# Optimization experiments

Measured on AMD Instinct MI355X. Metric: run time of the kernel, lower is better.

The kernel has to match this reference:

```python
import jax, jax.numpy as jnp
import numpy as np

B, C, Q, E, H = 8, 1024, 128, 512, 1024


def setup_inputs() -> dict:
    key = jax.random.key(0)
    ks = jax.random.split(key, 8)
    return {
        "context": jax.random.normal(ks[0], (B, C, E), jnp.float32),
        "question": jax.random.normal(ks[1], (B, Q, E), jnp.float32),
        "context_mask": jnp.ones((B, C), jnp.float32),
        "w_question": jax.random.normal(ks[2], (E,), jnp.float32),
        "w_context": jax.random.normal(ks[3], (E,), jnp.float32),
        "w_multiple": jax.random.normal(ks[4], (E,), jnp.float32),
        "W1": jax.random.normal(ks[5], (4 * E, H), jnp.float32) * 0.02,
        "b1": jnp.zeros((H,), jnp.float32),
        "W2": jax.random.normal(ks[6], (H, 4 * E), jnp.float32) * 0.02,
        "b2": jnp.zeros((4 * E,), jnp.float32),
    }


def reference(context, question, context_mask, w_question, w_context, w_multiple, W1, b1, W2, b2):
    # Dropout is identity at eval time.
    # Trilinear similarity: s[b,c,q] = q.w_q + ctx.w_c + sum_e q_e*ctx_e*w_m_e
    q_w = question @ w_question                                  # (B,Q)
    c_w = context @ w_context                                    # (B,C)
    mult = jnp.einsum("bqe,bce->bcq", question * w_multiple, context)  # avoids (B,C,Q,E)
    sim = q_w[:, None, :] + c_w[:, :, None] + mult               # (B,C,Q)

    # Context2Query: softmax over question dim (dim=2)
    c2q = jnp.einsum("bcq,bqe->bce", jax.nn.softmax(sim, axis=2), question)
    # Query2Context: max over question dim, softmax over context dim (dim=1)
    q2c = jnp.einsum("bc,bce->be", jax.nn.softmax(jnp.max(sim, axis=2), axis=1), context)  # (B,E)

    attended = jnp.concatenate(
        [context, c2q, context * c2q, context * q2c[:, None, :]], axis=2
    )  # (B,C,4E)

    # MaskedLinear: linear then zero out masked context positions
    m = context_mask[:, :, None]
    h = (attended @ W1 + b1) * m
    out = jax.nn.relu((h @ W2 + b2) * m)
    return out
```

## Files before the change

### kernel.cpp

```cpp
#include <hip/hip_runtime.h>

typedef __bf16 bf16;
typedef __bf16 bf16x2 __attribute__((ext_vector_type(2)));
typedef __bf16 bf16x4 __attribute__((ext_vector_type(4)));
typedef __bf16 bf16x8 __attribute__((ext_vector_type(8)));
typedef float f32x4 __attribute__((ext_vector_type(4)));

#define AS1 __attribute__((address_space(1)))
#define AS3 __attribute__((address_space(3)))

__device__ __forceinline__ void async_copy16(const void* g, void* l) {
  __builtin_amdgcn_global_load_lds((const AS1 void*)g, (AS3 void*)l, 16, 0, 0);
}

#define BB 8
#define CC 1024
#define QQ 128
#define EE 512
#define HH 1024
#define FOURE 2048

__global__ __launch_bounds__(256) void prep_kernel(
    const float* __restrict__ W1, const float* __restrict__ W2,
    const float* __restrict__ qst, const float* __restrict__ wmul,
    const float* __restrict__ wqv, bf16* __restrict__ W1T,
    bf16* __restrict__ W2T, bf16* __restrict__ qT,
    bf16* __restrict__ qmh, bf16* __restrict__ qml, float* __restrict__ qw,
    float* __restrict__ q2c) {
  __shared__ float tile[32][33];
  __shared__ float r4[4];
  int bx = blockIdx.x;
  int t = threadIdx.x;
  if (bx >= 5120) {
    for (int i = t; i < BB * EE; i += 256) q2c[i] = 0.f;
    return;
  }
  if (bx >= 4608) {
    int i = bx - 4608;
    int half = t >> 7, tr = t & 127;
    int rowg = i * 2 + half;
    const float* qrow = qst + (size_t)rowg * EE;
    float4 qv = *(const float4*)&qrow[tr * 4];
    float4 wm4 = *(const float4*)&wmul[tr * 4];
    float4 wq4 = *(const float4*)&wqv[tr * 4];
    float m[4] = {qv.x * wm4.x, qv.y * wm4.y, qv.z * wm4.z, qv.w * wm4.w};
    bf16x4 h, l;
#pragma unroll
    for (int k = 0; k < 4; ++k) {
      bf16 hh = (bf16)m[k];
      h[k] = hh; l[k] = (bf16)(m[k] - (float)hh);
    }
    *(bf16x4*)&qmh[(size_t)rowg * EE + tr * 4] = h;
    *(bf16x4*)&qml[(size_t)rowg * EE + tr * 4] = l;
    float s = qv.x * wq4.x + qv.y * wq4.y + qv.z * wq4.z + qv.w * wq4.w;
#pragma unroll
    for (int off = 32; off; off >>= 1) s += __shfl_xor(s, off);
    if ((t & 63) == 0) r4[t >> 6] = s;
    __syncthreads();
    if (tr == 0) qw[rowg] = r4[half * 2] + r4[half * 2 + 1];
    return;
  }
  const float* src;
  bf16* dst;
  int R, C, idx;
  if (bx < 2048) {
    src = W1; dst = W1T; R = 2048; C = 1024; idx = bx;
  } else if (bx < 4096) {
    src = W2; dst = W2T; R = 1024; C = 2048; idx = bx - 2048;
  } else {
    int i = bx - 4096;
    int b = i >> 6; idx = i & 63;
    src = qst + (size_t)b * QQ * EE; dst = qT + (size_t)b * EE * QQ;
    R = 128; C = 512;
  }
  int ctiles = C >> 5;
  int by = idx / ctiles, cx = idx % ctiles;
  int tx = t & 31, ty = t >> 5;
#pragma unroll
  for (int rr = 0; rr < 4; ++rr)
    tile[ty + rr * 8][tx] = src[(size_t)(by * 32 + ty + rr * 8) * C + cx * 32 + tx];
  __syncthreads();
#pragma unroll
  for (int rr = 0; rr < 4; ++rr)
    dst[(size_t)(cx * 32 + ty + rr * 8) * R + by * 32 + tx] = (bf16)tile[tx][ty + rr * 8];
}

__global__ __launch_bounds__(256) void fused_att_kernel(
    const float* __restrict__ ctx, const bf16* __restrict__ qmh,
    const bf16* __restrict__ qml, const bf16* __restrict__ qT,
    const float* __restrict__ wc, const float* __restrict__ qw,
    float* __restrict__ smax, bf16* __restrict__ att) {
  int bid = blockIdx.x;
  int b = bid & 7;
  int m0 = (bid >> 3) * 16;
  __shared__ __align__(16) char U[26880];
  bf16* Ah = (bf16*)(U);
  bf16* Al = (bf16*)(U + 1024);
  bf16* Bh = (bf16*)(U + 2048);
  bf16* Bl = (bf16*)(U + 10240);
  float(*sim_s)[132] = (float(*)[132])(U + 18432);
  bf16* c2q_lds = (bf16*)(U);
  __shared__ float wc_s[EE];
  __shared__ float qw_s[QQ];
  __shared__ float cw_s[16];
  __shared__ bf16 P_lds[16][136];
  int t = threadIdx.x;
  for (int i = t; i < EE; i += 256) wc_s[i] = wc[i];
  if (t < QQ) qw_s[t] = qw[b * QQ + t];
  __syncthreads();
  int wv = t >> 6, ln = t & 63;
  int rl = ln & 15, kq = ln >> 4;
  f32x4 acc[2] = {};
  const float* Ag = ctx + ((size_t)b * CC + m0) * EE;
  const bf16* Bhg = qmh + (size_t)b * QQ * EE;
  const bf16* Blg = qml + (size_t)b * QQ * EE;
  int arow = t >> 4, ae = (t & 15) * 2;
  float cwp = 0.f;
  for (int k0 = 0; k0 < EE; k0 += 32) {
    {
      float2 v = *(const float2*)(Ag + (size_t)arow * EE + k0 + ae);
      cwp += v.x * wc_s[k0 + ae] + v.y * wc_s[k0 + ae + 1];
      bf16 h0 = (bf16)v.x, h1 = (bf16)v.y;
      bf16x2 h, l;
      h[0] = h0; h[1] = h1;
      l[0] = (bf16)(v.x - (float)h0);
      l[1] = (bf16)(v.y - (float)h1);
      int sl = ((ae >> 3) ^ ((arow >> 1) & 3)) * 8 + (ae & 7);
      *(bf16x2*)&Ah[arow * 32 + sl] = h;
      *(bf16x2*)&Al[arow * 32 + sl] = l;
    }
#pragma unroll
    for (int r = 0; r < 2; ++r) {
      int fb = (r * 4 + wv) * 1024 + ln * 16;
      int row = fb >> 6;
      int cq = ((fb >> 4) & 3) ^ ((row >> 1) & 3);
      async_copy16(Bhg + (size_t)row * EE + k0 + cq * 8, (char*)Bh + fb);
      async_copy16(Blg + (size_t)row * EE + k0 + cq * 8, (char*)Bl + fb);
    }
    __syncthreads();
    bf16x8 ah, al, bh[2], bl[2];
    {
      int sl = (kq ^ ((rl >> 1) & 3)) * 8;
      ah = *(const bf16x8*)&Ah[rl * 32 + sl];
      al = *(const bf16x8*)&Al[rl * 32 + sl];
    }
#pragma unroll
    for (int j = 0; j < 2; ++j) {
      int r = wv * 32 + j * 16 + rl;
      int sl = (kq ^ ((r >> 1) & 3)) * 8;
      bh[j] = *(const bf16x8*)&Bh[r * 32 + sl];
      bl[j] = *(const bf16x8*)&Bl[r * 32 + sl];
    }
#pragma unroll
    for (int j = 0; j < 2; ++j) {
      acc[j] = __builtin_amdgcn_mfma_f32_16x16x32_bf16(ah, bh[j], acc[j], 0, 0, 0);
      acc[j] = __builtin_amdgcn_mfma_f32_16x16x32_bf16(ah, bl[j], acc[j], 0, 0, 0);
      acc[j] = __builtin_amdgcn_mfma_f32_16x16x32_bf16(al, bh[j], acc[j], 0, 0, 0);
    }
    __syncthreads();
  }
  {
    float s = cwp;
    s += __shfl_xor(s, 1); s += __shfl_xor(s, 2);
    s += __shfl_xor(s, 4); s += __shfl_xor(s, 8);
    if ((t & 15) == 0) cw_s[arow] = s;
  }
#pragma unroll
  for (int j = 0; j < 2; ++j) {
    int col = wv * 32 + j * 16 + rl;
    float qv = qw_s[col];
    int rbase = kq * 4;
#pragma unroll
    for (int r = 0; r < 4; ++r) sim_s[rbase + r][col] = acc[j][r] + qv;
  }
  __syncthreads();
  {
    int row = t >> 4, cb = t & 15;
    float v[8];
    float mx = -3.4e38f;
#pragma unroll
    for (int k = 0; k < 8; ++k) {
      v[k] = sim_s[row][cb + 16 * k];
      mx = fmaxf(mx, v[k]);
    }
    mx = fmaxf(mx, __shfl_xor(mx, 1));
    mx = fmaxf(mx, __shfl_xor(mx, 2));
    mx = fmaxf(mx, __shfl_xor(mx, 4));
    mx = fmaxf(mx, __shfl_xor(mx, 8));
    float sm = 0.f;
#pragma unroll
    for (int k = 0; k < 8; ++k) { v[k] = __expf(v[k] - mx); sm += v[k]; }
    sm += __shfl_xor(sm, 1);
    sm += __shfl_xor(sm, 2);
    sm += __shfl_xor(sm, 4);
    sm += __shfl_xor(sm, 8);
    float inv = 1.0f / sm;
#pragma unroll
    for (int k = 0; k < 8; ++k) P_lds[row][cb + 16 * k] = (bf16)(v[k] * inv);
    if (cb == 0) smax[b * CC + m0 + row] = mx + cw_s[row];
  }
  __syncthreads();
  f32x4 acc2[8] = {};
  const bf16* qTb = qT + (size_t)b * EE * QQ;
#pragma unroll
  for (int kk = 0; kk < 4; ++kk) {
    bf16x8 af2;
    {
      bf16x4 lo = *(const bf16x4*)&P_lds[rl][kk * 32 + kq * 8];
      bf16x4 hi = *(const bf16x4*)&P_lds[rl][kk * 32 + kq * 8 + 4];
      af2[0] = lo[0]; af2[1] = lo[1]; af2[2] = lo[2]; af2[3] = lo[3];
      af2[4] = hi[0]; af2[5] = hi[1]; af2[6] = hi[2]; af2[7] = hi[3];
    }
#pragma unroll
    for (int j = 0; j < 8; ++j) {
      int n = wv * 128 + j * 16 + rl;
      bf16x8 bfr = *(const bf16x8*)&qTb[(size_t)n * QQ + kk * 32 + kq * 8];
      acc2[j] = __builtin_amdgcn_mfma_f32_16x16x32_bf16(af2, bfr, acc2[j], 0, 0, 0);
    }
  }
#pragma unroll
  for (int j = 0; j < 8; ++j) {
    int col = wv * 128 + j * 16 + rl;
    int rbase = kq * 4;
#pragma unroll
    for (int r = 0; r < 4; ++r)
      c2q_lds[(size_t)(rbase + r) * 520 + col] = (bf16)acc2[j][r];
  }
  __syncthreads();
  {
    int row = t >> 4, tc = t & 15;
    const float* crow = ctx + ((size_t)(b * CC + m0 + row)) * EE;
    bf16* arow_p = att + ((size_t)(b * CC + m0 + row)) * FOURE;
#pragma unroll
    for (int cc = 0; cc < 4; ++cc) {
      int col = cc * 128 + tc * 8;
      bf16x8 q8 = *(const bf16x8*)&c2q_lds[(size_t)row * 520 + col];
      float4 v0 = *(const float4*)&crow[col];
      float4 v1 = *(const float4*)&crow[col + 4];
      float cv[8] = {v0.x, v0.y, v0.z, v0.w, v1.x, v1.y, v1.z, v1.w};
      bf16x8 o0, o2;
#pragma unroll
      for (int k = 0; k < 8; ++k) {
        o0[k] = (bf16)cv[k];
        o2[k] = (bf16)(cv[k] * (float)q8[k]);
      }
      *(bf16x8*)&arow_p[col] = o0;
      *(bf16x8*)&arow_p[EE + col] = q8;
      *(bf16x8*)&arow_p[2 * EE + col] = o2;
    }
  }
}

__global__ __launch_bounds__(256) void q2c_kernel(
    const float* __restrict__ ctx, const float* __restrict__ smax,
    float* __restrict__ q2c) {
  int b = blockIdx.x & 7, ch = blockIdx.x >> 3;
  int t = threadIdx.x;
  __shared__ float red[256];
  __shared__ float w_s[32];
  float v[4];
  float mx = -3.4e38f;
#pragma unroll
  for (int i = 0; i < 4; ++i) {
    v[i] = smax[b * CC + i * 256 + t];
    mx = fmaxf(mx, v[i]);
  }
  red[t] = mx;
  __syncthreads();
  for (int s = 128; s > 0; s >>= 1) {
    if (t < s) red[t] = fmaxf(red[t], red[t + s]);
    __syncthreads();
  }
  mx = red[0];
  __syncthreads();
  float sm = 0.f;
#pragma unroll
  for (int i = 0; i < 4; ++i) sm += __expf(v[i] - mx);
  red[t] = sm;
  __syncthreads();
  for (int s = 128; s > 0; s >>= 1) {
    if (t < s) red[t] += red[t + s];
    __syncthreads();
  }
  float inv = 1.0f / red[0];
  if (t < 32) w_s[t] = __expf(smax[b * CC + ch * 32 + t] - mx) * inv;
  __syncthreads();
  int e = t * 2;
  const float* cb = ctx + ((size_t)b * CC + ch * 32) * EE;
  float a0 = 0.f, a1 = 0.f;
#pragma unroll 8
  for (int r = 0; r < 32; ++r) {
    float2 vv = *(const float2*)&cb[(size_t)r * EE + e];
    float w = w_s[r];
    a0 += w * vv.x;
    a1 += w * vv.y;
  }
  atomicAdd(&q2c[b * EE + e], a0);
  atomicAdd(&q2c[b * EE + e + 1], a1);
}

__global__ __launch_bounds__(256) void att3_kernel(
    const float* __restrict__ ctx, const float* __restrict__ q2c,
    bf16* __restrict__ att) {
  int b = blockIdx.x & 7;
  int inner = (blockIdx.x >> 3) * 256 + threadIdx.x;
  int row = b * CC + (inner >> 6);
  int e = (inner & 63) * 8;
  float4 v0 = *(const float4*)&ctx[(size_t)row * EE + e];
  float4 v1 = *(const float4*)&ctx[(size_t)row * EE + e + 4];
  float4 g0 = *(const float4*)&q2c[b * EE + e];
  float4 g1 = *(const float4*)&q2c[b * EE + e + 4];
  bf16x8 o;
  o[0] = (bf16)(v0.x * g0.x); o[1] = (bf16)(v0.y * g0.y);
  o[2] = (bf16)(v0.z * g0.z); o[3] = (bf16)(v0.w * g0.w);
  o[4] = (bf16)(v1.x * g1.x); o[5] = (bf16)(v1.y * g1.y);
  o[6] = (bf16)(v1.z * g1.z); o[7] = (bf16)(v1.w * g1.w);
  *(bf16x8*)&att[(size_t)row * FOURE + 3 * EE + e] = o;
}

template <int OUT_BF16, int RELU>
__global__ __launch_bounds__(512, 2) void gemm_bt_p2_kernel(
    const bf16* __restrict__ A, const bf16* __restrict__ Bt,
    const float* __restrict__ bias, const float* __restrict__ mask,
    void* __restrict__ Cout, int M, int N, int K) {
  __shared__ bf16 As[3][256 * 64];
  __shared__ bf16 Bs[3][128 * 64];
  int ntiles = N >> 7;
  int tiles_per_g = 8 * ntiles;
  int g = blockIdx.x / tiles_per_g, sub = blockIdx.x % tiles_per_g;
  int mt = g * 8 + (sub & 7), ntb = sub >> 3;
  int m0 = mt << 8, n0 = ntb << 7;
  int t = threadIdx.x, wv = t >> 6, ln = t & 63;
  int wm = wv >> 1, wn = wv & 1;
  int rl = ln & 15, kq = ln >> 4;
  int NT = K >> 6;

  auto stageA = [&](int buf, int kt, int r) {
    int k0 = kt << 6;
    int fb = r * 8192 + t * 16;
    int row = fb >> 7;
    int q = ((fb >> 4) & 7) ^ (row & 7);
    async_copy16(A + (size_t)(m0 + row) * K + k0 + q * 8, (char*)As[buf] + fb);
  };
  auto stageB = [&](int buf, int kt, int r) {
    int k0 = kt << 6;
    int fb = r * 8192 + t * 16;
    int row = fb >> 7;
    int q = ((fb >> 4) & 7) ^ (row & 7);
    async_copy16(Bt + (size_t)(n0 + row) * K + k0 + q * 8, (char*)Bs[buf] + fb);
  };

#pragma unroll
  for (int r = 0; r < 4; ++r) stageA(0, 0, r);
#pragma unroll
  for (int r = 0; r < 2; ++r) stageB(0, 0, r);
#pragma unroll
  for (int r = 0; r < 4; ++r) stageA(1, 1, r);
#pragma unroll
  for (int r = 0; r < 2; ++r) stageB(1, 1, r);
  asm volatile("s_waitcnt vmcnt(6)" ::: "memory");
  __builtin_amdgcn_s_barrier();

  f32x4 acc[4][4] = {};
  int cur = 0;
  for (int kt = 0; kt < NT; ++kt) {
    const bf16* Ab = As[cur];
    const bf16* Bb = Bs[cur];
    int nxt = cur + 2; if (nxt >= 3) nxt -= 3;
    bool pf = (kt + 2) < NT;
    bf16x8 af0[2][2], bfr[2][4];
#pragma unroll
    for (int ks = 0; ks < 2; ++ks) {
      int c = ks * 4 + kq;
#pragma unroll
      for (int i = 0; i < 2; ++i) {
        int row = wm * 64 + i * 16 + rl;
        af0[ks][i] = *(const bf16x8*)&Ab[row * 64 + ((c ^ (row & 7)) * 8)];
      }
#pragma unroll
      for (int j = 0; j < 4; ++j) {
        int row = wn * 64 + j * 16 + rl;
        bfr[ks][j] = *(const bf16x8*)&Bb[row * 64 + ((c ^ (row & 7)) * 8)];
      }
    }
    if (pf) { stageA(nxt, kt + 2, 0); stageA(nxt, kt + 2, 1); stageA(nxt, kt + 2, 2); }
    __builtin_amdgcn_s_barrier();
    asm volatile("s_waitcnt lgkmcnt(0)" ::: "memory");
    __builtin_amdgcn_sched_barrier(0);
    __builtin_amdgcn_s_setprio(1);
#pragma unroll
    for (int ks = 0; ks < 2; ++ks)
#pragma unroll
      for (int i = 0; i < 2; ++i)
#pragma unroll
        for (int j = 0; j < 4; ++j)
          acc[i][j] = __builtin_amdgcn_mfma_f32_16x16x32_bf16(
              af0[ks][i], bfr[ks][j], acc[i][j], 0, 0, 0);
    __builtin_amdgcn_s_setprio(0);
    __builtin_amdgcn_s_barrier();
    bf16x8 af1[2][2];
#pragma unroll
    for (int ks = 0; ks < 2; ++ks) {
      int c = ks * 4 + kq;
#pragma unroll
      for (int i = 0; i < 2; ++i) {
        int row = wm * 64 + (i + 2) * 16 + rl;
        af1[ks][i] = *(const bf16x8*)&Ab[row * 64 + ((c ^ (row & 7)) * 8)];
      }
    }
    if (pf) { stageA(nxt, kt + 2, 3); stageB(nxt, kt + 2, 0); stageB(nxt, kt + 2, 1); }
    __builtin_amdgcn_s_barrier();
    asm volatile("s_waitcnt lgkmcnt(0)" ::: "memory");
    __builtin_amdgcn_sched_barrier(0);
    __builtin_amdgcn_s_setprio(1);
#pragma unroll
    for (int ks = 0; ks < 2; ++ks)
#pragma unroll
      for (int i = 0; i < 2; ++i)
#pragma unroll
        for (int j = 0; j < 4; ++j)
          acc[i + 2][j] = __builtin_amdgcn_mfma_f32_16x16x32_bf16(
              af1[ks][i], bfr[ks][j], acc[i + 2][j], 0, 0, 0);
    __builtin_amdgcn_s_setprio(0);
    if (kt + 1 < NT) {
      if (pf) asm volatile("s_waitcnt vmcnt(6)" ::: "memory");
      else    asm volatile("s_waitcnt vmcnt(0)" ::: "memory");
      __builtin_amdgcn_s_barrier();
    }
    cur += 1; if (cur >= 3) cur -= 3;
  }

  float bv4[4];
#pragma unroll
  for (int j = 0; j < 4; ++j) bv4[j] = bias[n0 + wn * 64 + j * 16 + rl];
#pragma unroll
  for (int i = 0; i < 4; ++i) {
    int rbase = m0 + wm * 64 + i * 16 + (kq << 2);
#pragma unroll
    for (int r = 0; r < 4; ++r) {
      int row = rbase + r;
      float mk = mask[row];
#pragma unroll
      for (int j = 0; j < 4; ++j) {
        int col = n0 + wn * 64 + j * 16 + rl;
        float v = acc[i][j][r] + bv4[j];
        v *= mk;
        if (RELU) v = fmaxf(v, 0.f);
        if (OUT_BF16)
          ((bf16*)Cout)[(size_t)row * N + col] = (bf16)v;
        else
          ((float*)Cout)[(size_t)row * N + col] = v;
      }
    }
  }
}

template <int OUT_BF16, int RELU>
__global__ __launch_bounds__(512, 2) void gemm_ph8_kernel(
    const bf16* __restrict__ A, const bf16* __restrict__ Bt,
    const float* __restrict__ bias, const float* __restrict__ mask,
    void* __restrict__ Cout, int M, int N, int K) {
  __shared__ bf16 As[2][256 * 64];
  __shared__ bf16 Bs[2][256 * 64];
  int ntn = N >> 8;
  int nblk = (M >> 8) * ntn;
  int cpx = nblk >> 3;
  int swz = (blockIdx.x & 7) * cpx + (blockIdx.x >> 3);
  int mt = swz / ntn, ntb = swz % ntn;
  int m0 = mt << 8, n0 = ntb << 8;
  int t = threadIdx.x, wv = t >> 6, ln = t & 63;
  int wm = wv >> 2, wn = wv & 3;
  int rl = ln & 15, kq = ln >> 4;
  int NT = K >> 6;
  int chunk = t & 7;

  auto stage = [&](int buf, int k1, int arr, int half, int r) {
    int fb = r * 8192 + t * 16;
    int phys = half * 128 + (fb >> 7);
    int q = chunk ^ (phys & 7);
    if (arr == 0) {
      int lg = ((phys >> 6) & 1) * 128 + (phys >> 7) * 64 + (phys & 63);
      async_copy16(A + (size_t)(m0 + lg) * K + k1 + q * 8,
                   (char*)&As[buf][0] + half * 16384 + fb);
    } else {
      int lg = ((phys >> 5) & 3) * 64 + (phys >> 7) * 32 + (phys & 31);
      async_copy16(Bt + (size_t)(n0 + lg) * K + k1 + q * 8,
                   (char*)&Bs[buf][0] + half * 16384 + fb);
    }
  };
  auto ldA = [&](const bf16* Ab, int i, int ks) {
    int pr = (i >> 2) * 128 + wm * 64 + (i & 3) * 16 + rl;
    return *(const bf16x8*)&Ab[pr * 64 + (((ks * 4 + kq) ^ (pr & 7)) * 8)];
  };
  auto ldB = [&](const bf16* Bb, int j, int ks) {
    int pr = (j >> 1) * 128 + wn * 32 + (j & 1) * 16 + rl;
    return *(const bf16x8*)&Bb[pr * 64 + (((ks * 4 + kq) ^ (pr & 7)) * 8)];
  };

  stage(0, 0, 0, 0, 0); stage(0, 0, 0, 0, 1);
  stage(0, 0, 1, 0, 0); stage(0, 0, 1, 0, 1);
  stage(0, 0, 0, 1, 0); stage(0, 0, 0, 1, 1);
  stage(0, 0, 1, 1, 0); stage(0, 0, 1, 1, 1);
  stage(1, 64, 0, 0, 0); stage(1, 64, 0, 0, 1);
  stage(1, 64, 1, 0, 0); stage(1, 64, 1, 0, 1);
  asm volatile("s_waitcnt vmcnt(4)" ::: "memory");
  __builtin_amdgcn_s_barrier();

  f32x4 acc[8][4] = {};
  bf16x8 aX[4][2], bL[2][2], bH[2][2];
  int NI = NT >> 1;
  for (int it = 0; it < NI; ++it) {
    const bf16* A0 = &As[0][0];
    const bf16* B0 = &Bs[0][0];
    const bf16* A1 = &As[1][0];
    const bf16* B1 = &Bs[1][0];
    int t1k = ((it << 1) + 1) << 6;
    int t2k = ((it << 1) + 2) << 6;
    int t3k = ((it << 1) + 3) << 6;
    bool s2 = ((it << 1) + 2) < NT;
    bool s3 = ((it << 1) + 3) < NT;
    bool last = (it == NI - 1);

#pragma unroll
    for (int i = 0; i < 4; ++i) { aX[i][0] = ldA(A0, i, 0); aX[i][1] = ldA(A0, i, 1); }
#pragma unroll
    for (int j = 0; j < 2; ++j) { bL[j][0] = ldB(B0, j, 0); bL[j][1] = ldB(B0, j, 1); }
    stage(1, t1k, 0, 1, 0); stage(1, t1k, 0, 1, 1);
    asm volatile("s_waitcnt lgkmcnt(8)" ::: "memory");
    __builtin_amdgcn_s_barrier();
    asm volatile("s_waitcnt lgkmcnt(0)" ::: "memory");
    __builtin_amdgcn_sched_barrier(0);
    __builtin_amdgcn_s_setprio(1);
#pragma unroll
    for (int ks = 0; ks < 2; ++ks)
#pragma unroll
      for (int i = 0; i < 4; ++i)
#pragma unroll
        for (int j = 0; j < 2; ++j)
          acc[i][j] = __builtin_amdgcn_mfma_f32_16x16x32_bf16(
              aX[i][ks], bL[j][ks], acc[i][j], 0, 0, 0);
    __builtin_amdgcn_s_setprio(0);
    __builtin_amdgcn_s_barrier();
#pragma unroll
    for (int j = 0; j < 2; ++j) { bH[j][0] = ldB(B0, j + 2, 0); bH[j][1] = ldB(B0, j + 2, 1); }
    stage(1, t1k, 1, 1, 0); stage(1, t1k, 1, 1, 1);
    __builtin_amdgcn_s_barrier();
    asm volatile("s_waitcnt lgkmcnt(0)" ::: "memory");
    __builtin_amdgcn_sched_barrier(0);
    __builtin_amdgcn_s_setprio(1);
#pragma unroll
    for (int ks = 0; ks < 2; ++ks)
#pragma unroll
      for (int i = 0; i < 4; ++i)
#pragma unroll
        for (int j = 0; j < 2; ++j)
          acc[i][j + 2] = __builtin_amdgcn_mfma_f32_16x16x32_bf16(
              aX[i][ks], bH[j][ks], acc[i][j + 2], 0, 0, 0);
    __builtin_amdgcn_s_setprio(0);
    __builtin_amdgcn_s_barrier();
#pragma unroll
    for (int i = 0; i < 4; ++i) { aX[i][0] = ldA(A0, i + 4, 0); aX[i][1] = ldA(A0, i + 4, 1); }
    if (s2) { stage(0, t2k, 0, 0, 0); stage(0, t2k, 0, 0, 1); }
    __builtin_amdgcn_s_barrier();
    asm volatile("s_waitcnt lgkmcnt(0)" ::: "memory");
    __builtin_amdgcn_sched_barrier(0);
    __builtin_amdgcn_s_setprio(1);
#pragma unroll
    for (int ks = 0; ks < 2; ++ks)
#pragma unroll
      for (int i = 0; i < 4; ++i)
#pragma unroll
        for (int j = 0; j < 2; ++j)
          acc[i + 4][j] = __builtin_amdgcn_mfma_f32_16x16x32_bf16(
              aX[i][ks], bL[j][ks], acc[i + 4][j], 0, 0, 0);
    __builtin_amdgcn_s_setprio(0);
    __builtin_amdgcn_s_barrier();
    if (s2) { stage(0, t2k, 1, 0, 0); stage(0, t2k, 1, 0, 1); }
    __builtin_amdgcn_s_barrier();
    __builtin_amdgcn_s_setprio(1);
#pragma unroll
    for (int ks = 0; ks < 2; ++ks)
#pragma unroll
      for (int i = 0; i < 4; ++i)
#pragma unroll
        for (int j = 0; j < 2; ++j)
          acc[i + 4][j + 2] = __builtin_amdgcn_mfma_f32_16x16x32_bf16(
              aX[i][ks], bH[j][ks], acc[i + 4][j + 2], 0, 0, 0);
    __builtin_amdgcn_s_setprio(0);
    if (last) asm volatile("s_waitcnt vmcnt(0)" ::: "memory");
    else      asm volatile("s_waitcnt vmcnt(4)" ::: "memory");
    __builtin_amdgcn_s_barrier();
#pragma unroll
    for (int i = 0; i < 4; ++i) { aX[i][0] = ldA(A1, i, 0); aX[i][1] = ldA(A1, i, 1); }
#pragma unroll
    for (int j = 0; j < 2; ++j) { bL[j][0] = ldB(B1, j, 0); bL[j][1] = ldB(B1, j, 1); }
    if (s2) { stage(0, t2k, 0, 1, 0); stage(0, t2k, 0, 1, 1); }
    asm volatile("s_waitcnt lgkmcnt(8)" ::: "memory");
    __builtin_amdgcn_s_barrier();
    asm volatile("s_waitcnt lgkmcnt(0)" ::: "memory");
    __builtin_amdgcn_sched_barrier(0);
    __builtin_amdgcn_s_setprio(1);
#pragma unroll
    for (int ks = 0; ks < 2; ++ks)
#pragma unroll
      for (int i = 0; i < 4; ++i)
#pragma unroll
        for (int j = 0; j < 2; ++j)
          acc[i][j] = __builtin_amdgcn_mfma_f32_16x16x32_bf16(
              aX[i][ks], bL[j][ks], acc[i][j], 0, 0, 0);
    __builtin_amdgcn_s_setprio(0);
    __builtin_amdgcn_s_barrier();
#pragma unroll
    for (int j = 0; j < 2; ++j) { bH[j][0] = ldB(B1, j + 2, 0); bH[j][1] = ldB(B1, j + 2, 1); }
    if (s2) { stage(0, t2k, 1, 1, 0); stage(0, t2k, 1, 1, 1); }
    __builtin_amdgcn_s_barrier();
    asm volatile("s_waitcnt lgkmcnt(0)" ::: "memory");
    __builtin_amdgcn_sched_barrier(0);
    __builtin_amdgcn_s_setprio(1);
#pragma unroll
    for (int ks = 0; ks < 2; ++ks)
#pragma unroll
      for (int i = 0; i < 4; ++i)
#pragma unroll
        for (int j = 0; j < 2; ++j)
          acc[i][j + 2] = __builtin_amdgcn_mfma_f32_16x16x32_bf16(
              aX[i][ks], bH[j][ks], acc[i][j + 2], 0, 0, 0);
    __builtin_amdgcn_s_setprio(0);
    __builtin_amdgcn_s_barrier();
#pragma unroll
    for (int i = 0; i < 4; ++i) { aX[i][0] = ldA(A1, i + 4, 0); aX[i][1] = ldA(A1, i + 4, 1); }
    if (s3) { stage(1, t3k, 0, 0, 0); stage(1, t3k, 0, 0, 1); }
    __builtin_amdgcn_s_barrier();
    asm volatile("s_waitcnt lgkmcnt(0)" ::: "memory");
    __builtin_amdgcn_sched_barrier(0);
    __builtin_amdgcn_s_setprio(1);
#pragma unroll
    for (int ks = 0; ks < 2; ++ks)
#pragma unroll
      for (int i = 0; i < 4; ++i)
#pragma unroll
        for (int j = 0; j < 2; ++j)
          acc[i + 4][j] = __builtin_amdgcn_mfma_f32_16x16x32_bf16(
              aX[i][ks], bL[j][ks], acc[i + 4][j], 0, 0, 0);
    __builtin_amdgcn_s_setprio(0);
    __builtin_amdgcn_s_barrier();
    if (s3) { stage(1, t3k, 1, 0, 0); stage(1, t3k, 1, 0, 1); }
    __builtin_amdgcn_s_barrier();
    __builtin_amdgcn_s_setprio(1);
#pragma unroll
    for (int ks = 0; ks < 2; ++ks)
#pragma unroll
      for (int i = 0; i < 4; ++i)
#pragma unroll
        for (int j = 0; j < 2; ++j)
          acc[i + 4][j + 2] = __builtin_amdgcn_mfma_f32_16x16x32_bf16(
              aX[i][ks], bH[j][ks], acc[i + 4][j + 2], 0, 0, 0);
    __builtin_amdgcn_s_setprio(0);
    if (!last) {
      asm volatile("s_waitcnt vmcnt(4)" ::: "memory");
      __builtin_amdgcn_s_barrier();
    }
  }

  float bv4[4];
#pragma unroll
  for (int j = 0; j < 4; ++j) bv4[j] = bias[n0 + wn * 64 + j * 16 + rl];
#pragma unroll
  for (int i = 0; i < 8; ++i) {
    int rbase = m0 + wm * 128 + i * 16 + (kq << 2);
#pragma unroll
    for (int r = 0; r < 4; ++r) {
      int row = rbase + r;
      float mk = mask[row];
#pragma unroll
      for (int j = 0; j < 4; ++j) {
        int col = n0 + wn * 64 + j * 16 + rl;
        float v = acc[i][j][r] + bv4[j];
        v *= mk;
        if (RELU) v = fmaxf(v, 0.f);
        if (OUT_BF16)
          ((bf16*)Cout)[(size_t)row * N + col] = (bf16)v;
        else
          ((float*)Cout)[(size_t)row * N + col] = v;
      }
    }
  }
}

extern "C" void kernel_launch(void* const* d_in, const int* in_sizes, int n_in,
                              void* d_out, int out_size, void* d_ws, size_t ws_size,
                              hipStream_t stream) {
  const float* ctx = (const float*)d_in[0];
  const float* qst = (const float*)d_in[1];
  const float* mask = (const float*)d_in[2];
  const float* wqv = (const float*)d_in[3];
  const float* wcv = (const float*)d_in[4];
  const float* wmul = (const float*)d_in[5];
  const float* W1 = (const float*)d_in[6];
  const float* b1 = (const float*)d_in[7];
  const float* W2 = (const float*)d_in[8];
  const float* b2 = (const float*)d_in[9];
  float* out = (float*)d_out;
  char* ws = (char*)d_ws;

  bf16* att = (bf16*)(ws);
  bf16* hbuf = (bf16*)(ws + 33554432);
  bf16* W1T = (bf16*)(ws + 50331648);
  bf16* W2T = (bf16*)(ws + 54525952);
  bf16* qT = (bf16*)(ws + 58720256);
  bf16* qmh = (bf16*)(ws + 59768832);
  bf16* qml = (bf16*)(ws + 60817408);
  float* smax = (float*)(ws + 61865984);
  float* q2c = (float*)(ws + 61898752);
  float* qw = (float*)(ws + 61915136);

  prep_kernel<<<5121, 256, 0, stream>>>(W1, W2, qst, wmul, wqv,
                                        W1T, W2T, qT, qmh, qml, qw, q2c);
  fused_att_kernel<<<512, 256, 0, stream>>>(ctx, qmh, qml, qT, wcv,
                                            qw, smax, att);
  q2c_kernel<<<256, 256, 0, stream>>>(ctx, smax, q2c);
  att3_kernel<<<2048, 256, 0, stream>>>(ctx, q2c, att);
  gemm_bt_p2_kernel<1, 0><<<256, 512, 0, stream>>>(
      att, W1T, b1, mask, hbuf, 8192, 1024, 2048);
  gemm_ph8_kernel<0, 1><<<256, 512, 0, stream>>>(
      hbuf, W2T, b2, mask, out, 8192, 2048, 1024);
}
```

Before: 214.8 us.

## Overlap weight transposes with attention kernel and double-buffer B tiles

After: 217.5 us. Within noise of the previous version (+1.3%).

```diff
diff --git a/kernel.cpp b/kernel.cpp
--- a/kernel.cpp
+++ b/kernel.cpp
@@ -21,22 +21,20 @@
 #define FOURE 2048
 
 __global__ __launch_bounds__(256) void prep_kernel(
-    const float* __restrict__ W1, const float* __restrict__ W2,
     const float* __restrict__ qst, const float* __restrict__ wmul,
-    const float* __restrict__ wqv, bf16* __restrict__ W1T,
-    bf16* __restrict__ W2T, bf16* __restrict__ qT,
+    const float* __restrict__ wqv, bf16* __restrict__ qT,
     bf16* __restrict__ qmh, bf16* __restrict__ qml, float* __restrict__ qw,
     float* __restrict__ q2c) {
   __shared__ float tile[32][33];
   __shared__ float r4[4];
   int bx = blockIdx.x;
   int t = threadIdx.x;
-  if (bx >= 5120) {
+  if (bx >= 1024) {
     for (int i = t; i < BB * EE; i += 256) q2c[i] = 0.f;
     return;
   }
-  if (bx >= 4608) {
-    int i = bx - 4608;
+  if (bx >= 512) {
+    int i = bx - 512;
     int half = t >> 7, tr = t & 127;
     int rowg = i * 2 + half;
     const float* qrow = qst + (size_t)rowg * EE;
@@ -60,96 +58,113 @@
     if (tr == 0) qw[rowg] = r4[half * 2] + r4[half * 2 + 1];
     return;
   }
-  const float* src;
-  bf16* dst;
-  int R, C, idx;
-  if (bx < 2048) {
-    src = W1; dst = W1T; R = 2048; C = 1024; idx = bx;
-  } else if (bx < 4096) {
-    src = W2; dst = W2T; R = 1024; C = 2048; idx = bx - 2048;
-  } else {
-    int i = bx - 4096;
-    int b = i >> 6; idx = i & 63;
-    src = qst + (size_t)b * QQ * EE; dst = qT + (size_t)b * EE * QQ;
-    R = 128; C = 512;
-  }
-  int ctiles = C >> 5;
-  int by = idx / ctiles, cx = idx % ctiles;
+  int b = bx >> 6, idx = bx & 63;
+  const float* src = qst + (size_t)b * QQ * EE;
+  bf16* dst = qT + (size_t)b * EE * QQ;
+  int by = idx / 16, cx = idx % 16;
   int tx = t & 31, ty = t >> 5;
 #pragma unroll
   for (int rr = 0; rr < 4; ++rr)
-    tile[ty + rr * 8][tx] = src[(size_t)(by * 32 + ty + rr * 8) * C + cx * 32 + tx];
+    tile[ty + rr * 8][tx] = src[(size_t)(by * 32 + ty + rr * 8) * EE + cx * 32 + tx];
   __syncthreads();
 #pragma unroll
   for (int rr = 0; rr < 4; ++rr)
-    dst[(size_t)(cx * 32 + ty + rr * 8) * R + by * 32 + tx] = (bf16)tile[tx][ty + rr * 8];
+    dst[(size_t)(cx * 32 + ty + rr * 8) * QQ + by * 32 + tx] = (bf16)tile[tx][ty + rr * 8];
 }
 
 __global__ __launch_bounds__(256) void fused_att_kernel(
     const float* __restrict__ ctx, const bf16* __restrict__ qmh,
     const bf16* __restrict__ qml, const bf16* __restrict__ qT,
     const float* __restrict__ wc, const float* __restrict__ qw,
-    float* __restrict__ smax, bf16* __restrict__ att) {
-  int bid = blockIdx.x;
-  int b = bid & 7;
-  int m0 = (bid >> 3) * 16;
-  __shared__ __align__(16) char U[26880];
-  bf16* Ah = (bf16*)(U);
-  bf16* Al = (bf16*)(U + 1024);
-  bf16* Bh = (bf16*)(U + 2048);
-  bf16* Bl = (bf16*)(U + 10240);
-  float(*sim_s)[132] = (float(*)[132])(U + 18432);
-  bf16* c2q_lds = (bf16*)(U);
+    float* __restrict__ smax, bf16* __restrict__ att,
+    const float* __restrict__ W1, const float* __restrict__ W2,
+    bf16* __restrict__ W1T, bf16* __restrict__ W2T) {
+  __shared__ __align__(16) char U[32768];
   __shared__ float wc_s[EE];
   __shared__ float qw_s[QQ];
   __shared__ float cw_s[16];
   __shared__ bf16 P_lds[16][136];
+  int bid = blockIdx.x;
   int t = threadIdx.x;
+  if (bid >= 512) {
+    float(*tile)[33] = (float(*)[33])U;
+    int tid = bid - 512;
+    const float* src; bf16* dst; int R, C;
+    if (tid < 2048) { src = W1; dst = W1T; R = 2048; C = 1024; }
+    else            { src = W2; dst = W2T; R = 1024; C = 2048; tid -= 2048; }
+    int ctiles = C >> 5;
+    int by = tid / ctiles, cx = tid % ctiles;
+    int tx = t & 31, ty = t >> 5;
+#pragma unroll
+    for (int rr = 0; rr < 4; ++rr)
+      tile[ty + rr * 8][tx] = src[(size_t)(by * 32 + ty + rr * 8) * C + cx * 32 + tx];
+    __syncthreads();
+#pragma unroll
+    for (int rr = 0; rr < 4; ++rr)
+      dst[(size_t)(cx * 32 + ty + rr * 8) * R + by * 32 + tx] = (bf16)tile[tx][ty + rr * 8];
+    return;
+  }
+  int b = bid & 7;
+  int m0 = (bid >> 3) * 16;
+  bf16* Bh = (bf16*)(U);
+  bf16* Bl = (bf16*)(U + 16384);
+  float(*sim_s)[132] = (float(*)[132])(U);
+  bf16* c2q_lds = (bf16*)(U);
   for (int i = t; i < EE; i += 256) wc_s[i] = wc[i];
   if (t < QQ) qw_s[t] = qw[b * QQ + t];
-  __syncthreads();
   int wv = t >> 6, ln = t & 63;
   int rl = ln & 15, kq = ln >> 4;
-  f32x4 acc[2] = {};
   const float* Ag = ctx + ((size_t)b * CC + m0) * EE;
   const bf16* Bhg = qmh + (size_t)b * QQ * EE;
   const bf16* Blg = qml + (size_t)b * QQ * EE;
-  int arow = t >> 4, ae = (t & 15) * 2;
+#pragma unroll
+  for (int r = 0; r < 2; ++r) {
+    int fb = (r * 4 + wv) * 1024 + ln * 16;
+    int row = fb >> 6;
+    int cq = ((fb >> 4) & 3) ^ ((row >> 1) & 3);
+    async_copy16(Bhg + (size_t)row * EE + cq * 8, (char*)Bh + fb);
+    async_copy16(Blg + (size_t)row * EE + cq * 8, (char*)Bl + fb);
+  }
+  __syncthreads();
+  f32x4 acc[2] = {};
   float cwp = 0.f;
-  for (int k0 = 0; k0 < EE; k0 += 32) {
-    {
-      float2 v = *(const float2*)(Ag + (size_t)arow * EE + k0 + ae);
-      cwp += v.x * wc_s[k0 + ae] + v.y * wc_s[k0 + ae + 1];
-      bf16 h0 = (bf16)v.x, h1 = (bf16)v.y;
-      bf16x2 h, l;
-      h[0] = h0; h[1] = h1;
-      l[0] = (bf16)(v.x - (float)h0);
-      l[1] = (bf16)(v.y - (float)h1);
-      int sl = ((ae >> 3) ^ ((arow >> 1) & 3)) * 8 + (ae & 7);
-      *(bf16x2*)&Ah[arow * 32 + sl] = h;
-      *(bf16x2*)&Al[arow * 32 + sl] = l;
-    }
-#pragma unroll
-    for (int r = 0; r < 2; ++r) {
-      int fb = (r * 4 + wv) * 1024 + ln * 16;
-      int row = fb >> 6;
-      int cq = ((fb >> 4) & 3) ^ ((row >> 1) & 3);
-      async_copy16(Bhg + (size_t)row * EE + k0 + cq * 8, (char*)Bh + fb);
-      async_copy16(Blg + (size_t)row * EE + k0 + cq * 8, (char*)Bl + fb);
-    }
-    __syncthreads();
-    bf16x8 ah, al, bh[2], bl[2];
-    {
-      int sl = (kq ^ ((rl >> 1) & 3)) * 8;
-      ah = *(const bf16x8*)&Ah[rl * 32 + sl];
-      al = *(const bf16x8*)&Al[rl * 32 + sl];
-    }
+  for (int it = 0; it < 16; ++it) {
+    int k0 = it * 32;
+    int cur = (it & 1) * 8192;
+    int nxt = 8192 - cur;
+    if (it + 1 < 16) {
+#pragma unroll
+      for (int r = 0; r < 2; ++r) {
+        int fb = (r * 4 + wv) * 1024 + ln * 16;
+        int row = fb >> 6;
+        int cq = ((fb >> 4) & 3) ^ ((row >> 1) & 3);
+        async_copy16(Bhg + (size_t)row * EE + k0 + 32 + cq * 8,
+                     (char*)Bh + nxt + fb);
+        async_copy16(Blg + (size_t)row * EE + k0 + 32 + cq * 8,
+                     (char*)Bl + nxt + fb);
+      }
+    }
+    const float* ap = Ag + (size_t)rl * EE + k0 + kq * 8;
+    float4 a0 = *(const float4*)ap;
+    float4 a1 = *(const float4*)(ap + 4);
+    float av[8] = {a0.x, a0.y, a0.z, a0.w, a1.x, a1.y, a1.z, a1.w};
+    bf16x8 ah, al;
+#pragma unroll
+    for (int k = 0; k < 8; ++k) {
+      bf16 hh = (bf16)av[k];
+      ah[k] = hh; al[k] = (bf16)(av[k] - (float)hh);
+    }
+    if (wv == 0) {
+#pragma unroll
+      for (int k = 0; k < 8; ++k) cwp += av[k] * wc_s[k0 + kq * 8 + k];
+    }
+    bf16x8 bh[2], bl[2];
 #pragma unroll
     for (int j = 0; j < 2; ++j) {
       int r = wv * 32 + j * 16 + rl;
       int sl = (kq ^ ((r >> 1) & 3)) * 8;
-      bh[j] = *(const bf16x8*)&Bh[r * 32 + sl];
-      bl[j] = *(const bf16x8*)&Bl[r * 32 + sl];
+      bh[j] = *(const bf16x8*)((const char*)Bh + cur + (r * 32 + sl) * 2);
+      bl[j] = *(const bf16x8*)((const char*)Bl + cur + (r * 32 + sl) * 2);
     }
 #pragma unroll
     for (int j = 0; j < 2; ++j) {
@@ -159,11 +174,11 @@
     }
     __syncthreads();
   }
-  {
+  if (wv == 0) {
     float s = cwp;
-    s += __shfl_xor(s, 1); s += __shfl_xor(s, 2);
-    s += __shfl_xor(s, 4); s += __shfl_xor(s, 8);
-    if ((t & 15) == 0) cw_s[arow] = s;
+    s += __shfl_xor(s, 16);
+    s += __shfl_xor(s, 32);
+    if (ln < 16) cw_s[ln] = s;
   }
 #pragma unroll
   for (int j = 0; j < 2; ++j) {
@@ -256,7 +271,7 @@
     float* __restrict__ q2c) {
   int b = blockIdx.x & 7, ch = blockIdx.x >> 3;
   int t = threadIdx.x;
-  __shared__ float red[256];
+  __shared__ float red4m[4], red4s[4];
   __shared__ float w_s[32];
   float v[4];
   float mx = -3.4e38f;
@@ -265,24 +280,19 @@
     v[i] = smax[b * CC + i * 256 + t];
     mx = fmaxf(mx, v[i]);
   }
-  red[t] = mx;
+#pragma unroll
+  for (int off = 32; off; off >>= 1) mx = fmaxf(mx, __shfl_xor(mx, off));
+  if ((t & 63) == 0) red4m[t >> 6] = mx;
   __syncthreads();
-  for (int s = 128; s > 0; s >>= 1) {
-    if (t < s) red[t] = fmaxf(red[t], red[t + s]);
-    __syncthreads();
-  }
-  mx = red[0];
+  mx = fmaxf(fmaxf(red4m[0], red4m[1]), fmaxf(red4m[2], red4m[3]));
+  float sm = 0.f;
+#pragma unroll
+  for (int i = 0; i < 4; ++i) sm += __expf(v[i] - mx);
+#pragma unroll
+  for (int off = 32; off; off >>= 1) sm += __shfl_xor(sm, off);
+  if ((t & 63) == 0) red4s[t >> 6] = sm;
   __syncthreads();
-  float sm = 0.f;
-#pragma unroll
-  for (int i = 0; i < 4; ++i) sm += __expf(v[i] - mx);
-  red[t] = sm;
-  __syncthreads();
-  for (int s = 128; s > 0; s >>= 1) {
-    if (t < s) red[t] += red[t + s];
-    __syncthreads();
-  }
-  float inv = 1.0f / red[0];
+  float inv = 1.0f / (red4s[0] + red4s[1] + red4s[2] + red4s[3]);
   if (t < 32) w_s[t] = __expf(smax[b * CC + ch * 32 + t] - mx) * inv;
   __syncthreads();
   int e = t * 2;
@@ -714,10 +724,9 @@
   float* q2c = (float*)(ws + 61898752);
   float* qw = (float*)(ws + 61915136);
 
-  prep_kernel<<<5121, 256, 0, stream>>>(W1, W2, qst, wmul, wqv,
-                                        W1T, W2T, qT, qmh, qml, qw, q2c);
-  fused_att_kernel<<<512, 256, 0, stream>>>(ctx, qmh, qml, qT, wcv,
-                                            qw, smax, att);
+  prep_kernel<<<1025, 256, 0, stream>>>(qst, wmul, wqv, qT, qmh, qml, qw, q2c);
+  fused_att_kernel<<<4608, 256, 0, stream>>>(ctx, qmh, qml, qT, wcv, qw,
+                                             smax, att, W1, W2, W1T, W2T);
   q2c_kernel<<<256, 256, 0, stream>>>(ctx, smax, q2c);
   att3_kernel<<<2048, 256, 0, stream>>>(ctx, q2c, att);
   gemm_bt_p2_kernel<1, 0><<<256, 512, 0, stream>>>(
```
